# Optimization experiments

Measured on AMD Instinct MI355X. Metric: run time of the kernel, lower is better.

## Reference

```python
import jax, jax.numpy as jnp
import numpy as np

N = 20000
E_RAND = 320000
NEG_SLOPE = 0.2


def setup_inputs() -> dict:
    key = jax.random.key(0)
    ks = jax.random.split(key, 10)
    x = jax.random.normal(ks[0], (N, 768), dtype=jnp.float32)
    src = jax.random.randint(ks[1], (E_RAND,), 0, N)
    dst = jax.random.randint(ks[2], (E_RAND,), 0, N)
    loop = jnp.arange(N)
    edge_index = jnp.stack([jnp.concatenate([src, loop]),
                            jnp.concatenate([dst, loop])])  # [2, 340000]
    s = 1.0 / np.sqrt(768.0)
    W1 = jax.random.normal(ks[3], (768, 768), dtype=jnp.float32) * s
    a_src1 = jax.random.normal(ks[4], (8, 96), dtype=jnp.float32) * 0.1
    a_dst1 = jax.random.normal(ks[5], (8, 96), dtype=jnp.float32) * 0.1
    b1 = jnp.zeros((768,), dtype=jnp.float32)
    W2 = jax.random.normal(ks[6], (768, 768), dtype=jnp.float32) * s
    a_src2 = jax.random.normal(ks[7], (1, 768), dtype=jnp.float32) * 0.1
    a_dst2 = jax.random.normal(ks[8], (1, 768), dtype=jnp.float32) * 0.1
    b2 = jnp.zeros((768,), dtype=jnp.float32)
    return {"x": x, "edge_index": edge_index, "W1": W1, "a_src1": a_src1,
            "a_dst1": a_dst1, "b1": b1, "W2": W2, "a_src2": a_src2,
            "a_dst2": a_dst2, "b2": b2}


def gat_layer(x, W, a_src, a_dst, bias, src, dst, heads, out_c, concat):
    n = x.shape[0]
    h = (x @ W).reshape(n, heads, out_c)                      # [N,H,C]
    al_s = jnp.einsum('nhc,hc->nh', h, a_src)                 # [N,H]
    al_d = jnp.einsum('nhc,hc->nh', h, a_dst)
    e = jax.nn.leaky_relu(al_s[src] + al_d[dst], NEG_SLOPE)   # [E,H]
    m = jax.ops.segment_max(e, dst, num_segments=n)           # segment softmax
    ex = jnp.exp(e - m[dst])
    z = jax.ops.segment_sum(ex, dst, num_segments=n)
    alpha = ex / (z[dst] + 1e-16)                             # [E,H]
    msg = h[src] * alpha[:, :, None]                          # [E,H,C]
    out = jax.ops.segment_sum(msg, dst, num_segments=n)       # [N,H,C]
    out = out.reshape(n, heads * out_c) if concat else out.mean(axis=1)
    return out + bias


def reference(x, edge_index, W1, a_src1, a_dst1, b1, W2, a_src2, a_dst2, b2):
    src, dst = edge_index[0], edge_index[1]
    h = gat_layer(x, W1, a_src1, a_dst1, b1, src, dst, heads=8, out_c=96, concat=True)
    h = jax.nn.elu(h)
    out = gat_layer(h, W2, a_src2, a_dst2, b2, src, dst, heads=1, out_c=768, concat=False)
    return out
```

## Files before the change

### kernel.cpp

```cpp
#include <hip/hip_runtime.h>
#include <cstdint>
#include <cstddef>

typedef _Float16 f16;
typedef _Float16 f16x4 __attribute__((ext_vector_type(4)));
typedef _Float16 f16x8 __attribute__((ext_vector_type(8)));
typedef float f32x4 __attribute__((ext_vector_type(4)));

#define LRELU_SLOPE 0.2f

#define GLL16(g, l)                                                          \
  __builtin_amdgcn_global_load_lds(                                          \
      (const __attribute__((address_space(1))) void*)(g),                    \
      (__attribute__((address_space(3))) void*)(l), 16, 0, 0)

__global__ __launch_bounds__(256) void k_prep_xh(const float* __restrict__ x,
                                                 f16* __restrict__ xh,
                                                 int nvalid, int npad) {
  int total = npad * 192;
  for (int idx = blockIdx.x * blockDim.x + threadIdx.x; idx < total;
       idx += gridDim.x * blockDim.x) {
    int row = idx / 192;
    f16x4 o;
    if (row < nvalid) {
      const float4 v = *(const float4*)(x + (size_t)idx * 4);
      o[0] = (f16)v.x; o[1] = (f16)v.y; o[2] = (f16)v.z; o[3] = (f16)v.w;
    } else {
      o[0] = (f16)0.f; o[1] = (f16)0.f; o[2] = (f16)0.f; o[3] = (f16)0.f;
    }
    *(f16x4*)(xh + (size_t)idx * 4) = o;
  }
}

__global__ __launch_bounds__(256) void k_transpose_w2(const float* __restrict__ W1,
                                                      const float* __restrict__ W2,
                                                      f16* __restrict__ Wt1,
                                                      f16* __restrict__ Wt2) {
  const float* W = blockIdx.z ? W2 : W1;
  f16* Wt = blockIdx.z ? Wt2 : Wt1;
  __shared__ float tile[32][33];
  int bn = blockIdx.x * 32;
  int bk = blockIdx.y * 32;
  int tx = threadIdx.x & 31, ty = threadIdx.x >> 5;
  #pragma unroll
  for (int r = ty; r < 32; r += 8)
    tile[r][tx] = W[(size_t)(bk + r) * 768 + bn + tx];
  __syncthreads();
  #pragma unroll
  for (int r = ty; r < 32; r += 8)
    Wt[(size_t)(bn + r) * 768 + bk + tx] = (f16)tile[tx][r];
}

__global__ void k_hist(const int* __restrict__ dst, int E, int* __restrict__ counts) {
  for (int e = blockIdx.x * blockDim.x + threadIdx.x; e < E;
       e += gridDim.x * blockDim.x) atomicAdd(&counts[dst[e]], 1);
}

__global__ __launch_bounds__(1024) void k_scan_block(const int* __restrict__ counts,
                                                     int* __restrict__ starts,
                                                     int* __restrict__ cursor, int n) {
  const int t = threadIdx.x;
  const int nthr = 1024;
  const int chunk = (n + nthr - 1) / nthr;
  const int base = t * chunk;
  int tsum = 0;
  for (int i = 0; i < chunk; i++) {
    int idx = base + i;
    if (idx < n) tsum += counts[idx];
  }
  int lane = t & 63, wv = t >> 6;
  int s = tsum;
  #pragma unroll
  for (int off = 1; off < 64; off <<= 1) {
    int tmp = __shfl_up(s, off);
    if (lane >= off) s += tmp;
  }
  __shared__ int wsum[16];
  if (lane == 63) wsum[wv] = s;
  __syncthreads();
  int woff = 0;
  for (int w = 0; w < wv; w++) woff += wsum[w];
  int run = woff + s - tsum;
  for (int i = 0; i < chunk; i++) {
    int idx = base + i;
    if (idx < n) {
      starts[idx] = run;
      cursor[idx] = run;
      run += counts[idx];
    }
  }
  if (t == nthr - 1) starts[n] = run;
}

__global__ void k_fill(const int* __restrict__ src, const int* __restrict__ dst, int E,
                       int* __restrict__ cursor, int* __restrict__ src_sorted) {
  for (int e = blockIdx.x * blockDim.x + threadIdx.x; e < E;
       e += gridDim.x * blockDim.x) {
    int slot = atomicAdd(&cursor[dst[e]], 1);
    src_sorted[slot] = src[e];
  }
}

__global__ __launch_bounds__(256) void k_gemm_f16(const f16* __restrict__ A,
                                                  const f16* __restrict__ Bt,
                                                  f16* __restrict__ C, int Mvalid) {
  __shared__ __align__(16) f16 As[8192];
  __shared__ __align__(16) f16 Bs[8192];
  const int K = 768;
  const int tid = threadIdx.x;
  const int bm = blockIdx.x * 128;
  const int bn = blockIdx.y * 128;
  const int lane = tid & 63;
  const int wave = tid >> 6;
  const int wr = (wave >> 1) * 64;
  const int wc = (wave & 1) * 64;

  size_t goffA[4], goffB[4];
  #pragma unroll
  for (int p = 0; p < 4; p++) {
    const int cell = p * 256 + tid;
    const int row = cell >> 3;
    const int cl = (cell & 7) ^ (row & 7);
    goffA[p] = (size_t)(bm + row) * K + cl * 8;
    goffB[p] = (size_t)(bn + row) * K + cl * 8;
  }

  f32x4 acc[4][4];
  const f32x4 vzero = {0.f, 0.f, 0.f, 0.f};
  #pragma unroll
  for (int i = 0; i < 4; i++)
    #pragma unroll
    for (int j = 0; j < 4; j++) acc[i][j] = vzero;

  const int fr = lane & 15;
  const int fq = lane >> 4;

  for (int k0 = 0; k0 < K; k0 += 64) {
    #pragma unroll
    for (int p = 0; p < 4; p++) GLL16(A + goffA[p] + k0, As + p * 2048 + wave * 512);
    #pragma unroll
    for (int p = 0; p < 4; p++) GLL16(Bt + goffB[p] + k0, Bs + p * 2048 + wave * 512);
    __syncthreads();
    #pragma unroll
    for (int ks = 0; ks < 2; ks++) {
      f16x8 af[4], bf[4];
      #pragma unroll
      for (int i = 0; i < 4; i++) {
        const int r = wr + i * 16 + fr;
        const int phys = (ks * 4 + fq) ^ (r & 7);
        af[i] = *(const f16x8*)(&As[r * 64 + phys * 8]);
      }
      #pragma unroll
      for (int j = 0; j < 4; j++) {
        const int r = wc + j * 16 + fr;
        const int phys = (ks * 4 + fq) ^ (r & 7);
        bf[j] = *(const f16x8*)(&Bs[r * 64 + phys * 8]);
      }
      #pragma unroll
      for (int i = 0; i < 4; i++)
        #pragma unroll
        for (int j = 0; j < 4; j++)
          acc[i][j] = __builtin_amdgcn_mfma_f32_16x16x32_f16(af[i], bf[j], acc[i][j], 0, 0, 0);
    }
    __syncthreads();
  }

  #pragma unroll
  for (int i = 0; i < 4; i++) {
    #pragma unroll
    for (int j = 0; j < 4; j++) {
      const int col = bn + wc + j * 16 + fr;
      #pragma unroll
      for (int r = 0; r < 4; r++) {
        const int row = bm + wr + i * 16 + fq * 4 + r;
        if (row < Mvalid) C[(size_t)row * 768 + col] = (f16)acc[i][j][r];
      }
    }
  }
}

template <int H>
__global__ __launch_bounds__(256) void k_al(const f16* __restrict__ h,
                                            const float* __restrict__ a_src,
                                            const float* __restrict__ a_dst,
                                            float* __restrict__ als,
                                            float* __restrict__ ald, int N) {
  int node = blockIdx.x * 4 + (threadIdx.x >> 6);
  int lane = threadIdx.x & 63;
  if (node >= N) return;
  const f16x4* hp = (const f16x4*)(h + (size_t)node * 768 + lane * 12);
  float ss = 0.f, sd = 0.f;
  int cbase = lane * 12;
  #pragma unroll
  for (int q = 0; q < 3; q++) {
    f16x4 hv = hp[q];
    #pragma unroll
    for (int j = 0; j < 4; j++) {
      int c = cbase + q * 4 + j;
      float v = (float)hv[j];
      ss += v * a_src[c];
      sd += v * a_dst[c];
    }
  }
  const int red = (H == 8) ? 8 : 64;
  #pragma unroll
  for (int off = 1; off < red; off <<= 1) {
    ss += __shfl_xor(ss, off);
    sd += __shfl_xor(sd, off);
  }
  if (H == 8) {
    if ((lane & 7) == 0) {
      als[(size_t)node * 8 + (lane >> 3)] = ss;
      ald[(size_t)node * 8 + (lane >> 3)] = sd;
    }
  } else {
    if (lane == 0) { als[node] = ss; ald[node] = sd; }
  }
}

template <int H, bool FINAL>
__global__ __launch_bounds__(192) void k_aggregate(
    const f16* __restrict__ h, const float* __restrict__ als,
    const float* __restrict__ ald, const int* __restrict__ starts,
    const int* __restrict__ src_sorted, const float* __restrict__ bias,
    void* __restrict__ outv, int nvalid) {
  const int n = blockIdx.x;
  const int t = threadIdx.x;
  if (n >= nvalid) return;
  __shared__ float s_ex[256 * H];
  __shared__ int s_src[256];
  __shared__ float s_zp[3][H];
  const int start = starts[n];
  const int deg = starts[n + 1] - start;
  const int lane = t & 63, wv = t >> 6;
  const int hA = (H == 8) ? (t & 7) : 0;
  const int myh = (H == 8) ? (t / 24) : 0;
  const float ald_A = ald[(size_t)n * H + hA];

  float zpart = 0.f;
  float4 acc = {0.f, 0.f, 0.f, 0.f};

  for (int cb = 0; cb < deg; cb += 256) {
    const int cnt = min(256, deg - cb);
    for (int idx = t; idx < cnt * H; idx += 192) {
      const int e = (H == 8) ? (idx >> 3) : idx;
      const int s = src_sorted[start + cb + e];
      if (H == 1 || (idx & 7) == 0) s_src[e] = s;
      float v = als[(size_t)s * H + hA] + ald_A;
      v = v > 0.f ? v : LRELU_SLOPE * v;
      const float ex = __expf(v);
      s_ex[idx] = ex;
      zpart += ex;
    }
    __syncthreads();
    for (int e = 0; e < cnt; e++) {
      const f16x4 hv = *(const f16x4*)(h + (size_t)s_src[e] * 768 + 4 * t);
      const float a = s_ex[e * H + myh];
      acc.x += a * (float)hv[0];
      acc.y += a * (float)hv[1];
      acc.z += a * (float)hv[2];
      acc.w += a * (float)hv[3];
    }
    __syncthreads();
  }

  if (H == 8) {
    #pragma unroll
    for (int off = 8; off < 64; off <<= 1) zpart += __shfl_xor(zpart, off);
    if (lane < 8) s_zp[wv][lane] = zpart;
  } else {
    #pragma unroll
    for (int off = 1; off < 64; off <<= 1) zpart += __shfl_xor(zpart, off);
    if (lane == 0) s_zp[wv][0] = zpart;
  }
  __syncthreads();
  const float z = s_zp[0][myh] + s_zp[1][myh] + s_zp[2][myh];
  const float inv = 1.f / (z + 1e-16f);

  const float4 bv = *(const float4*)(bias + 4 * t);
  float v0 = acc.x * inv + bv.x;
  float v1 = acc.y * inv + bv.y;
  float v2 = acc.z * inv + bv.z;
  float v3 = acc.w * inv + bv.w;
  if (!FINAL) {
    v0 = v0 > 0.f ? v0 : expm1f(v0);
    v1 = v1 > 0.f ? v1 : expm1f(v1);
    v2 = v2 > 0.f ? v2 : expm1f(v2);
    v3 = v3 > 0.f ? v3 : expm1f(v3);
    f16x4 o;
    o[0] = (f16)v0; o[1] = (f16)v1; o[2] = (f16)v2; o[3] = (f16)v3;
    *(f16x4*)((f16*)outv + (size_t)n * 768 + 4 * t) = o;
  } else {
    float4 o = {v0, v1, v2, v3};
    *(float4*)((float*)outv + (size_t)n * 768 + 4 * t) = o;
  }
}

extern "C" void kernel_launch(void* const* d_in, const int* in_sizes, int n_in,
                              void* d_out, int out_size, void* d_ws, size_t ws_size,
                              hipStream_t stream) {
  const float* x   = (const float*)d_in[0];
  const int*   ei  = (const int*)d_in[1];
  const float* W1  = (const float*)d_in[2];
  const float* as1 = (const float*)d_in[3];
  const float* ad1 = (const float*)d_in[4];
  const float* b1  = (const float*)d_in[5];
  const float* W2  = (const float*)d_in[6];
  const float* as2 = (const float*)d_in[7];
  const float* ad2 = (const float*)d_in[8];
  const float* b2  = (const float*)d_in[9];

  const int N = in_sizes[0] / 768;
  const int E = in_sizes[1] / 2;
  const int Mpad = (N + 127) & ~127;
  const int* srcp = ei;
  const int* dstp = ei + E;

  char* p = (char*)d_ws;
  auto alloc = [&](size_t b) { char* r = p; p += (b + 255) & ~(size_t)255; return r; };
  f16*   bufX   = (f16*)alloc((size_t)Mpad * 768 * sizeof(f16));
  f16*   bufH   = (f16*)alloc((size_t)Mpad * 768 * sizeof(f16));
  f16*   Wt1    = (f16*)alloc((size_t)768 * 768 * sizeof(f16));
  f16*   Wt2    = (f16*)alloc((size_t)768 * 768 * sizeof(f16));
  float* als1   = (float*)alloc((size_t)N * 8 * sizeof(float));
  float* ald1   = (float*)alloc((size_t)N * 8 * sizeof(float));
  float* als2   = (float*)alloc((size_t)N * sizeof(float));
  float* ald2   = (float*)alloc((size_t)N * sizeof(float));
  int*   counts = (int*)alloc((size_t)N * sizeof(int));
  int*   starts = (int*)alloc(((size_t)N + 1) * sizeof(int));
  int*   cursor = (int*)alloc((size_t)N * sizeof(int));
  int*   srcs   = (int*)alloc((size_t)E * sizeof(int));

  hipMemsetAsync(counts, 0, (size_t)N * sizeof(int), stream);
  k_hist<<<dim3(512), dim3(256), 0, stream>>>(dstp, E, counts);
  k_scan_block<<<dim3(1), dim3(1024), 0, stream>>>(counts, starts, cursor, N);
  k_fill<<<dim3(512), dim3(256), 0, stream>>>(srcp, dstp, E, cursor, srcs);

  k_prep_xh<<<dim3(1024), dim3(256), 0, stream>>>(x, bufX, N, Mpad);
  k_transpose_w2<<<dim3(24, 24, 2), dim3(256), 0, stream>>>(W1, W2, Wt1, Wt2);

  k_gemm_f16<<<dim3(Mpad / 128, 6), dim3(256), 0, stream>>>(bufX, Wt1, bufH, N);
  k_al<8><<<dim3((N + 3) / 4), dim3(256), 0, stream>>>(bufH, as1, ad1, als1, ald1, N);
  k_aggregate<8, false><<<dim3(N), dim3(192), 0, stream>>>(bufH, als1, ald1, starts, srcs, b1, bufX, N);

  k_gemm_f16<<<dim3(Mpad / 128, 6), dim3(256), 0, stream>>>(bufX, Wt2, bufH, N);
  k_al<1><<<dim3((N + 3) / 4), dim3(256), 0, stream>>>(bufH, as2, ad2, als2, ald2, N);
  k_aggregate<1, true><<<dim3(N), dim3(192), 0, stream>>>(bufH, als2, ald2, starts, srcs, b2, d_out, N);
}
```

Before: 340.2 us.

## Fuse attention-logit dot products into GEMM epilogue and drop k_al kernels

New measurement: 379.8 us. 1.12x slower.

```diff
diff --git a/kernel.cpp b/kernel.cpp
--- a/kernel.cpp
+++ b/kernel.cpp
@@ -101,9 +101,15 @@
   }
 }
 
+template <int H>
 __global__ __launch_bounds__(256) void k_gemm_f16(const f16* __restrict__ A,
                                                   const f16* __restrict__ Bt,
-                                                  f16* __restrict__ C, int Mvalid) {
+                                                  f16* __restrict__ C,
+                                                  const float* __restrict__ a_src,
+                                                  const float* __restrict__ a_dst,
+                                                  float* __restrict__ als,
+                                                  float* __restrict__ ald,
+                                                  int Mvalid) {
   __shared__ __align__(16) f16 As[8192];
   __shared__ __align__(16) f16 Bs[8192];
   const int K = 768;
@@ -177,44 +183,41 @@
       }
     }
   }
-}
-
-template <int H>
-__global__ __launch_bounds__(256) void k_al(const f16* __restrict__ h,
-                                            const float* __restrict__ a_src,
-                                            const float* __restrict__ a_dst,
-                                            float* __restrict__ als,
-                                            float* __restrict__ ald, int N) {
-  int node = blockIdx.x * 4 + (threadIdx.x >> 6);
-  int lane = threadIdx.x & 63;
-  if (node >= N) return;
-  const f16x4* hp = (const f16x4*)(h + (size_t)node * 768 + lane * 12);
-  float ss = 0.f, sd = 0.f;
-  int cbase = lane * 12;
-  #pragma unroll
-  for (int q = 0; q < 3; q++) {
-    f16x4 hv = hp[q];
-    #pragma unroll
-    for (int j = 0; j < 4; j++) {
-      int c = cbase + q * 4 + j;
-      float v = (float)hv[j];
-      ss += v * a_src[c];
-      sd += v * a_dst[c];
-    }
-  }
-  const int red = (H == 8) ? 8 : 64;
-  #pragma unroll
-  for (int off = 1; off < red; off <<= 1) {
-    ss += __shfl_xor(ss, off);
-    sd += __shfl_xor(sd, off);
-  }
-  if (H == 8) {
-    if ((lane & 7) == 0) {
-      als[(size_t)node * 8 + (lane >> 3)] = ss;
-      ald[(size_t)node * 8 + (lane >> 3)] = sd;
-    }
-  } else {
-    if (lane == 0) { als[node] = ss; ald[node] = sd; }
+
+  const int hA = (H == 8) ? ((bn + wc) / 96) : 0;
+  const int hB = (H == 8) ? ((bn + wc + 63) / 96) : 0;
+  #pragma unroll
+  for (int i = 0; i < 4; i++) {
+    #pragma unroll
+    for (int r = 0; r < 4; r++) {
+      const int row = bm + wr + i * 16 + fq * 4 + r;
+      float sA = 0.f, dA = 0.f, sB = 0.f, dB = 0.f;
+      #pragma unroll
+      for (int j = 0; j < 4; j++) {
+        const int col = bn + wc + j * 16 + fr;
+        const float v = acc[i][j][r];
+        const float as = a_src[col], ad = a_dst[col];
+        if (H == 8 && (col / 96) != hA) { sB += v * as; dB += v * ad; }
+        else { sA += v * as; dA += v * ad; }
+      }
+      #pragma unroll
+      for (int off = 1; off < 16; off <<= 1) {
+        sA += __shfl_xor(sA, off);
+        dA += __shfl_xor(dA, off);
+        if (H == 8 && hB != hA) {
+          sB += __shfl_xor(sB, off);
+          dB += __shfl_xor(dB, off);
+        }
+      }
+      if (fr == 0 && row < Mvalid) {
+        atomicAdd(&als[(size_t)row * H + hA], sA);
+        atomicAdd(&ald[(size_t)row * H + hA], dA);
+        if (H == 8 && hB != hA) {
+          atomicAdd(&als[(size_t)row * H + hB], sB);
+          atomicAdd(&ald[(size_t)row * H + hB], dB);
+        }
+      }
+    }
   }
 }
 
@@ -223,8 +226,8 @@
     const f16* __restrict__ h, const float* __restrict__ als,
     const float* __restrict__ ald, const int* __restrict__ starts,
     const int* __restrict__ src_sorted, const float* __restrict__ bias,
-    void* __restrict__ outv, int nvalid) {
-  const int n = blockIdx.x;
+    void* __restrict__ outv, int nvalid, int nbase) {
+  const int n = nbase + blockIdx.x;
   const int t = threadIdx.x;
   if (n >= nvalid) return;
   __shared__ float s_ex[256 * H];
@@ -253,6 +256,7 @@
       zpart += ex;
     }
     __syncthreads();
+    #pragma unroll 4
     for (int e = 0; e < cnt; e++) {
       const f16x4 hv = *(const f16x4*)(h + (size_t)s_src[e] * 768 + 4 * t);
       const float a = s_ex[e * H + myh];
@@ -332,6 +336,8 @@
   int*   srcs   = (int*)alloc((size_t)E * sizeof(int));
 
   hipMemsetAsync(counts, 0, (size_t)N * sizeof(int), stream);
+  hipMemsetAsync(als1, 0, (size_t)((char*)(ald2 + N) - (char*)als1), stream);
+
   k_hist<<<dim3(512), dim3(256), 0, stream>>>(dstp, E, counts);
   k_scan_block<<<dim3(1), dim3(1024), 0, stream>>>(counts, starts, cursor, N);
   k_fill<<<dim3(512), dim3(256), 0, stream>>>(srcp, dstp, E, cursor, srcs);
@@ -339,11 +345,20 @@
   k_prep_xh<<<dim3(1024), dim3(256), 0, stream>>>(x, bufX, N, Mpad);
   k_transpose_w2<<<dim3(24, 24, 2), dim3(256), 0, stream>>>(W1, W2, Wt1, Wt2);
 
-  k_gemm_f16<<<dim3(Mpad / 128, 6), dim3(256), 0, stream>>>(bufX, Wt1, bufH, N);
-  k_al<8><<<dim3((N + 3) / 4), dim3(256), 0, stream>>>(bufH, as1, ad1, als1, ald1, N);
-  k_aggregate<8, false><<<dim3(N), dim3(192), 0, stream>>>(bufH, als1, ald1, starts, srcs, b1, bufX, N);
-
-  k_gemm_f16<<<dim3(Mpad / 128, 6), dim3(256), 0, stream>>>(bufX, Wt2, bufH, N);
-  k_al<1><<<dim3((N + 3) / 4), dim3(256), 0, stream>>>(bufH, as2, ad2, als2, ald2, N);
-  k_aggregate<1, true><<<dim3(N), dim3(192), 0, stream>>>(bufH, als2, ald2, starts, srcs, b2, d_out, N);
-}
+  const int nh1 = (N + 1) / 2;
+  const int nh2 = N - nh1;
+
+  k_gemm_f16<8><<<dim3(Mpad / 128, 6), dim3(256), 0, stream>>>(
+      bufX, Wt1, bufH, as1, ad1, als1, ald1, N);
+  k_aggregate<8, false><<<dim3(nh1), dim3(192), 0, stream>>>(
+      bufH, als1, ald1, starts, srcs, b1, bufX, N, 0);
+  k_aggregate<8, false><<<dim3(nh2), dim3(192), 0, stream>>>(
+      bufH, als1, ald1, starts, srcs, b1, bufX, N, nh1);
+
+  k_gemm_f16<1><<<dim3(Mpad / 128, 6), dim3(256), 0, stream>>>(
+      bufX, Wt2, bufH, as2, ad2, als2, ald2, N);
+  k_aggregate<1, true><<<dim3(nh1), dim3(192), 0, stream>>>(
+      bufH, als2, ald2, starts, srcs, b2, d_out, N, 0);
+  k_aggregate<1, true><<<dim3(nh2), dim3(192), 0, stream>>>(
+      bufH, als2, ald2, starts, srcs, b2, d_out, N, nh1);
+}
```

## Double-buffer GEMM LDS tiles and remap workgroups across XCDs

Applied to the files above, without the earlier changes.

Result: faster. 320.1 us (-5.9%).

```diff
diff --git a/kernel.cpp b/kernel.cpp
--- a/kernel.cpp
+++ b/kernel.cpp
@@ -104,12 +104,19 @@
 __global__ __launch_bounds__(256) void k_gemm_f16(const f16* __restrict__ A,
                                                   const f16* __restrict__ Bt,
                                                   f16* __restrict__ C, int Mvalid) {
-  __shared__ __align__(16) f16 As[8192];
-  __shared__ __align__(16) f16 Bs[8192];
+  __shared__ __align__(16) f16 As[2][8192];
+  __shared__ __align__(16) f16 Bs[2][8192];
   const int K = 768;
   const int tid = threadIdx.x;
-  const int bm = blockIdx.x * 128;
-  const int bn = blockIdx.y * 128;
+
+  const int nwg = gridDim.x;
+  const int orig = blockIdx.x;
+  const int q = nwg >> 3, r = nwg & 7;
+  const int xcd = orig & 7;
+  const int wgid = (xcd < r ? xcd * (q + 1) : r * (q + 1) + (xcd - r) * q) + (orig >> 3);
+  const int bm = (wgid / 6) * 128;
+  const int bn = (wgid - (wgid / 6) * 6) * 128;
+
   const int lane = tid & 63;
   const int wave = tid >> 6;
   const int wr = (wave >> 1) * 64;
@@ -135,26 +142,37 @@
   const int fr = lane & 15;
   const int fq = lane >> 4;
 
-  for (int k0 = 0; k0 < K; k0 += 64) {
-    #pragma unroll
-    for (int p = 0; p < 4; p++) GLL16(A + goffA[p] + k0, As + p * 2048 + wave * 512);
-    #pragma unroll
-    for (int p = 0; p < 4; p++) GLL16(Bt + goffB[p] + k0, Bs + p * 2048 + wave * 512);
-    __syncthreads();
+  #define STAGE(buf, k0)                                                      \
+    do {                                                                      \
+      _Pragma("unroll")                                                       \
+      for (int p = 0; p < 4; p++) {                                           \
+        GLL16(A + goffA[p] + (k0), &As[buf][p * 2048 + wave * 512]);          \
+        GLL16(Bt + goffB[p] + (k0), &Bs[buf][p * 2048 + wave * 512]);         \
+      }                                                                       \
+    } while (0)
+
+  STAGE(0, 0);
+  asm volatile("s_waitcnt vmcnt(0)" ::: "memory");
+  __builtin_amdgcn_s_barrier();
+
+  const int NT = K / 64;
+  int cur = 0;
+  for (int t = 0; t < NT; t++) {
+    if (t + 1 < NT) STAGE(cur ^ 1, (t + 1) * 64);
     #pragma unroll
     for (int ks = 0; ks < 2; ks++) {
       f16x8 af[4], bf[4];
       #pragma unroll
       for (int i = 0; i < 4; i++) {
-        const int r = wr + i * 16 + fr;
-        const int phys = (ks * 4 + fq) ^ (r & 7);
-        af[i] = *(const f16x8*)(&As[r * 64 + phys * 8]);
+        const int rr = wr + i * 16 + fr;
+        const int phys = (ks * 4 + fq) ^ (rr & 7);
+        af[i] = *(const f16x8*)(&As[cur][rr * 64 + phys * 8]);
       }
       #pragma unroll
       for (int j = 0; j < 4; j++) {
-        const int r = wc + j * 16 + fr;
-        const int phys = (ks * 4 + fq) ^ (r & 7);
-        bf[j] = *(const f16x8*)(&Bs[r * 64 + phys * 8]);
+        const int rr = wc + j * 16 + fr;
+        const int phys = (ks * 4 + fq) ^ (rr & 7);
+        bf[j] = *(const f16x8*)(&Bs[cur][rr * 64 + phys * 8]);
       }
       #pragma unroll
       for (int i = 0; i < 4; i++)
@@ -162,8 +180,11 @@
         for (int j = 0; j < 4; j++)
           acc[i][j] = __builtin_amdgcn_mfma_f32_16x16x32_f16(af[i], bf[j], acc[i][j], 0, 0, 0);
     }
-    __syncthreads();
-  }
+    asm volatile("s_waitcnt vmcnt(0)" ::: "memory");
+    __builtin_amdgcn_s_barrier();
+    cur ^= 1;
+  }
+  #undef STAGE
 
   #pragma unroll
   for (int i = 0; i < 4; i++) {
@@ -171,9 +192,9 @@
     for (int j = 0; j < 4; j++) {
       const int col = bn + wc + j * 16 + fr;
       #pragma unroll
-      for (int r = 0; r < 4; r++) {
-        const int row = bm + wr + i * 16 + fq * 4 + r;
-        if (row < Mvalid) C[(size_t)row * 768 + col] = (f16)acc[i][j][r];
+      for (int rg = 0; rg < 4; rg++) {
+        const int row = bm + wr + i * 16 + fq * 4 + rg;
+        if (row < Mvalid) C[(size_t)row * 768 + col] = (f16)acc[i][j][rg];
       }
     }
   }
@@ -339,11 +360,13 @@
   k_prep_xh<<<dim3(1024), dim3(256), 0, stream>>>(x, bufX, N, Mpad);
   k_transpose_w2<<<dim3(24, 24, 2), dim3(256), 0, stream>>>(W1, W2, Wt1, Wt2);
 
-  k_gemm_f16<<<dim3(Mpad / 128, 6), dim3(256), 0, stream>>>(bufX, Wt1, bufH, N);
+  const int nwg = (Mpad / 128) * 6;
+
+  k_gemm_f16<<<dim3(nwg), dim3(256), 0, stream>>>(bufX, Wt1, bufH, N);
   k_al<8><<<dim3((N + 3) / 4), dim3(256), 0, stream>>>(bufH, as1, ad1, als1, ald1, N);
   k_aggregate<8, false><<<dim3(N), dim3(192), 0, stream>>>(bufH, als1, ald1, starts, srcs, b1, bufX, N);
 
-  k_gemm_f16<<<dim3(Mpad / 128, 6), dim3(256), 0, stream>>>(bufX, Wt2, bufH, N);
+  k_gemm_f16<<<dim3(nwg), dim3(256), 0, stream>>>(bufX, Wt2, bufH, N);
   k_al<1><<<dim3((N + 3) / 4), dim3(256), 0, stream>>>(bufH, as2, ad2, als2, ald2, N);
   k_aggregate<1, true><<<dim3(N), dim3(192), 0, stream>>>(bufH, als2, ald2, starts, srcs, b2, d_out, N);
 }
```

## Restructure GEMM: stage B half-K in LDS, stream A from global, XCD-aware tile order

Applied to the files above, without the earlier changes.

After: 475.5 us. +39.8%, slower.

```diff
diff --git a/kernel.cpp b/kernel.cpp
--- a/kernel.cpp
+++ b/kernel.cpp
@@ -101,79 +101,86 @@
   }
 }
 
-__global__ __launch_bounds__(256) void k_gemm_f16(const f16* __restrict__ A,
-                                                  const f16* __restrict__ Bt,
-                                                  f16* __restrict__ C, int Mvalid) {
-  __shared__ __align__(16) f16 As[8192];
-  __shared__ __align__(16) f16 Bs[8192];
+__global__ __launch_bounds__(256, 3) void k_gemm_f16(const f16* __restrict__ A,
+                                                     const f16* __restrict__ Bt,
+                                                     f16* __restrict__ C, int Mvalid) {
+  __shared__ __align__(16) f16 Bs[48 * 64 * 8];
   const int K = 768;
   const int tid = threadIdx.x;
-  const int bm = blockIdx.x * 128;
-  const int bn = blockIdx.y * 128;
+
+  const int nwg = gridDim.x;
+  const int orig = blockIdx.x;
+  const int q = nwg >> 3, r = nwg & 7;
+  const int xcd = orig & 7;
+  const int wgid = (xcd < r ? xcd * (q + 1) : r * (q + 1) + (xcd - r) * q) + (orig >> 3);
+  const int bm = (wgid / 12) * 128;
+  const int bn = (wgid - (wgid / 12) * 12) * 64;
+
   const int lane = tid & 63;
   const int wave = tid >> 6;
   const int wr = (wave >> 1) * 64;
-  const int wc = (wave & 1) * 64;
-
-  size_t goffA[4], goffB[4];
-  #pragma unroll
-  for (int p = 0; p < 4; p++) {
-    const int cell = p * 256 + tid;
-    const int row = cell >> 3;
-    const int cl = (cell & 7) ^ (row & 7);
-    goffA[p] = (size_t)(bm + row) * K + cl * 8;
-    goffB[p] = (size_t)(bn + row) * K + cl * 8;
-  }
-
-  f32x4 acc[4][4];
-  const f32x4 vzero = {0.f, 0.f, 0.f, 0.f};
-  #pragma unroll
-  for (int i = 0; i < 4; i++)
-    #pragma unroll
-    for (int j = 0; j < 4; j++) acc[i][j] = vzero;
-
+  const int wc = (wave & 1) * 32;
   const int fr = lane & 15;
   const int fq = lane >> 4;
 
-  for (int k0 = 0; k0 < K; k0 += 64) {
-    #pragma unroll
-    for (int p = 0; p < 4; p++) GLL16(A + goffA[p] + k0, As + p * 2048 + wave * 512);
-    #pragma unroll
-    for (int p = 0; p < 4; p++) GLL16(Bt + goffB[p] + k0, Bs + p * 2048 + wave * 512);
+  size_t goffB[12];
+  #pragma unroll
+  for (int p = 0; p < 12; p++) {
+    const int cell = p * 256 + tid;
+    const int col = cell & 63;
+    const int kc = cell >> 6;
+    goffB[p] = (size_t)(bn + col) * K + kc * 8;
+  }
+
+  const f16* arow[4];
+  #pragma unroll
+  for (int i = 0; i < 4; i++)
+    arow[i] = A + (size_t)(bm + wr + i * 16 + fr) * K + fq * 8;
+
+  f32x4 acc[4][2];
+  const f32x4 vzero = {0.f, 0.f, 0.f, 0.f};
+  #pragma unroll
+  for (int i = 0; i < 4; i++)
+    #pragma unroll
+    for (int j = 0; j < 2; j++) acc[i][j] = vzero;
+
+  #pragma unroll
+  for (int ph = 0; ph < 2; ph++) {
+    if (ph) __syncthreads();
+    #pragma unroll
+    for (int p = 0; p < 12; p++)
+      GLL16(Bt + goffB[p] + ph * 384, Bs + (p * 256 + (tid & ~63)) * 8 + (lane)*8);
     __syncthreads();
-    #pragma unroll
-    for (int ks = 0; ks < 2; ks++) {
-      f16x8 af[4], bf[4];
+
+    #pragma unroll 2
+    for (int t = 0; t < 12; t++) {
+      f16x8 af[4], bf[2];
       #pragma unroll
-      for (int i = 0; i < 4; i++) {
-        const int r = wr + i * 16 + fr;
-        const int phys = (ks * 4 + fq) ^ (r & 7);
-        af[i] = *(const f16x8*)(&As[r * 64 + phys * 8]);
-      }
+      for (int i = 0; i < 4; i++)
+        af[i] = *(const f16x8*)(arow[i] + ph * 384 + t * 32);
       #pragma unroll
-      for (int j = 0; j < 4; j++) {
-        const int r = wc + j * 16 + fr;
-        const int phys = (ks * 4 + fq) ^ (r & 7);
-        bf[j] = *(const f16x8*)(&Bs[r * 64 + phys * 8]);
+      for (int j = 0; j < 2; j++) {
+        const int col = wc + j * 16 + fr;
+        const int kc = t * 4 + fq;
+        bf[j] = *(const f16x8*)(&Bs[(kc * 64 + col) * 8]);
       }
       #pragma unroll
       for (int i = 0; i < 4; i++)
         #pragma unroll
-        for (int j = 0; j < 4; j++)
+        for (int j = 0; j < 2; j++)
           acc[i][j] = __builtin_amdgcn_mfma_f32_16x16x32_f16(af[i], bf[j], acc[i][j], 0, 0, 0);
     }
-    __syncthreads();
   }
 
   #pragma unroll
   for (int i = 0; i < 4; i++) {
     #pragma unroll
-    for (int j = 0; j < 4; j++) {
+    for (int j = 0; j < 2; j++) {
       const int col = bn + wc + j * 16 + fr;
       #pragma unroll
-      for (int r = 0; r < 4; r++) {
-        const int row = bm + wr + i * 16 + fq * 4 + r;
-        if (row < Mvalid) C[(size_t)row * 768 + col] = (f16)acc[i][j][r];
+      for (int rg = 0; rg < 4; rg++) {
+        const int row = bm + wr + i * 16 + fq * 4 + rg;
+        if (row < Mvalid) C[(size_t)row * 768 + col] = (f16)acc[i][j][rg];
       }
     }
   }
@@ -339,11 +346,13 @@
   k_prep_xh<<<dim3(1024), dim3(256), 0, stream>>>(x, bufX, N, Mpad);
   k_transpose_w2<<<dim3(24, 24, 2), dim3(256), 0, stream>>>(W1, W2, Wt1, Wt2);
 
-  k_gemm_f16<<<dim3(Mpad / 128, 6), dim3(256), 0, stream>>>(bufX, Wt1, bufH, N);
+  const int nwg = (Mpad / 128) * 12;
+
+  k_gemm_f16<<<dim3(nwg), dim3(256), 0, stream>>>(bufX, Wt1, bufH, N);
   k_al<8><<<dim3((N + 3) / 4), dim3(256), 0, stream>>>(bufH, as1, ad1, als1, ald1, N);
   k_aggregate<8, false><<<dim3(N), dim3(192), 0, stream>>>(bufH, als1, ald1, starts, srcs, b1, bufX, N);
 
-  k_gemm_f16<<<dim3(Mpad / 128, 6), dim3(256), 0, stream>>>(bufX, Wt2, bufH, N);
+  k_gemm_f16<<<dim3(nwg), dim3(256), 0, stream>>>(bufX, Wt2, bufH, N);
   k_al<1><<<dim3((N + 3) / 4), dim3(256), 0, stream>>>(bufH, as2, ad2, als2, ald2, N);
   k_aggregate<1, true><<<dim3(N), dim3(192), 0, stream>>>(bufH, als2, ald2, starts, srcs, b2, d_out, N);
 }
```
